# Performance work log

Hardware: AMD Instinct MI355X
Metric: run time of the kernel (lower is better)

Reference implementation:

```python
import jax, jax.numpy as jnp
import numpy as np

B, C, H, W = 2, 512, 48, 48
HEADS = 8
REDUCTION = 4
DPH = max(C // REDUCTION // HEADS, 1)   # 16
TOTAL = DPH * HEADS                      # 128
EPS_NORM = 1e-12
EPS_BN = 1e-5


def setup_inputs() -> dict:
    key = jax.random.key(0)
    ks = jax.random.split(key, 6)
    x = jax.random.normal(ks[0], (B, C, H, W), dtype=jnp.float32)
    # 1x1 convs stored as [out_ch, in_ch] matrices
    w_qkv = jax.random.normal(ks[1], (3 * TOTAL, C), dtype=jnp.float32) * (1.0 / np.sqrt(C))
    w_out = jax.random.normal(ks[2], (C, TOTAL), dtype=jnp.float32) * (1.0 / np.sqrt(TOTAL))
    temperature = jnp.ones((HEADS, 1, 1), dtype=jnp.float32)
    bn_gamma = jnp.ones((C,), dtype=jnp.float32)
    bn_beta = jnp.zeros((C,), dtype=jnp.float32)
    return {"x": x, "w_qkv": w_qkv, "temperature": temperature,
            "w_out": w_out, "bn_gamma": bn_gamma, "bn_beta": bn_beta}


def _l2norm(t):
    # F.normalize(t, dim=-1): t / max(||t||_2, eps)
    n = jnp.sqrt(jnp.sum(t * t, axis=-1, keepdims=True))
    return t / jnp.maximum(n, EPS_NORM)


def reference(x, w_qkv, temperature, w_out, bn_gamma, bn_beta):
    b, c, h, w = x.shape
    n = h * w
    # qkv 1x1 conv: [b, 3*TOTAL, h, w]
    qkv = jnp.einsum('bchw,oc->bohw', x, w_qkv)
    q, k, v = jnp.split(qkv, 3, axis=1)
    # [b, heads, dph, n] -> [b, heads, n, dph]
    def heads_tokens(t):
        return t.reshape(b, HEADS, DPH, n).transpose(0, 1, 3, 2)
    q = _l2norm(heads_tokens(q))
    k = _l2norm(heads_tokens(k))
    v = heads_tokens(v)
    # [b, heads, n, n]
    attn = jnp.einsum('bhnd,bhmd->bhnm', q, k) * temperature[None]
    attn = jax.nn.softmax(attn, axis=-1)
    out = jnp.einsum('bhnm,bhmd->bhnd', attn, v)          # [b, heads, n, dph]
    out = out.transpose(0, 1, 3, 2).reshape(b, TOTAL, h, w)
    # project_out: 1x1 conv then BatchNorm2d (training-mode batch stats)
    out = jnp.einsum('bthw,ct->bchw', out, w_out)
    mean = jnp.mean(out, axis=(0, 2, 3))
    var = jnp.mean((out - mean[None, :, None, None]) ** 2, axis=(0, 2, 3))
    out = (out - mean[None, :, None, None]) * jax.lax.rsqrt(var + EPS_BN)[None, :, None, None]
    out = out * bn_gamma[None, :, None, None] + bn_beta[None, :, None, None]
    return out
```

## Files before the change

kernel.cpp:

```cpp
#include <hip/hip_runtime.h>

#define NB 2
#define CC 512
#define NN 2304
#define NH 8
#define DD 16
#define TT 128
#define O3 384

typedef __attribute__((ext_vector_type(4))) float f32x4;
typedef __attribute__((ext_vector_type(8))) __bf16 bf16x8;
typedef __attribute__((ext_vector_type(4))) __bf16 bf16x4;
typedef __attribute__((ext_vector_type(4))) _Float16 f16x4;

__global__ __launch_bounds__(256) void k0_convert(
    const float* __restrict__ x, const float* __restrict__ wqkv,
    const float* __restrict__ wout,
    __bf16* __restrict__ xT, __bf16* __restrict__ wqb, __bf16* __restrict__ wob)
{
    int bid = blockIdx.x;
    int t = threadIdx.x;
    if (bid < 576) {
        __shared__ float tile[64][65];
        int b = bid / 288, rem = bid % 288;
        int nt = rem / 8, cb = rem % 8;
        int n0 = nt * 64, c0 = cb * 64;
        int tc = t >> 6, tn = t & 63;
#pragma unroll
        for (int i = 0; i < 16; i++) {
            int cl = i * 4 + tc;
            tile[cl][tn] = x[(size_t)(b * CC + c0 + cl) * NN + n0 + tn];
        }
        __syncthreads();
#pragma unroll
        for (int i = 0; i < 16; i++) {
            int nl = i * 4 + tc;
            xT[(size_t)(b * NN + n0 + nl) * CC + c0 + tn] = (__bf16)tile[tn][nl];
        }
    } else {
        int wid = bid - 576;
        int base = wid * 256 + t;
#pragma unroll
        for (int i = 0; i < 16; i++) {
            int j = base + i * 16384;
            if (j < O3 * CC) wqb[j] = (__bf16)wqkv[j];
            else             wob[j - O3 * CC] = (__bf16)wout[j - O3 * CC];
        }
    }
}

__global__ __launch_bounds__(256) void k1_qkv(
    const __bf16* __restrict__ xT, const __bf16* __restrict__ wqb,
    _Float16* __restrict__ Q, _Float16* __restrict__ K, _Float16* __restrict__ VT)
{
    int ob = blockIdx.x, nt = blockIdx.y, b = blockIdx.z;
    int lane = threadIdx.x & 63, wave = threadIdx.x >> 6;
    int quad = lane >> 4, col = lane & 15;
    int n0 = nt * 64 + wave * 16;
    int o0 = ob * 32;

    f32x4 acc[2];
    acc[0] = (f32x4){0.f, 0.f, 0.f, 0.f};
    acc[1] = (f32x4){0.f, 0.f, 0.f, 0.f};

    const __bf16* arow = xT + (size_t)(b * NN + n0 + col) * CC + quad * 8;
    const __bf16* brow0 = wqb + (size_t)(o0 + col) * CC + quad * 8;
    const __bf16* brow1 = brow0 + 16 * CC;

    bf16x8 a  = *(const bf16x8*)(arow);
    bf16x8 w0 = *(const bf16x8*)(brow0);
    bf16x8 w1 = *(const bf16x8*)(brow1);
#pragma unroll
    for (int ks = 0; ks < 16; ks++) {
        bf16x8 an, wn0, wn1;
        if (ks < 15) {
            an  = *(const bf16x8*)(arow + (ks + 1) * 32);
            wn0 = *(const bf16x8*)(brow0 + (ks + 1) * 32);
            wn1 = *(const bf16x8*)(brow1 + (ks + 1) * 32);
        }
        acc[0] = __builtin_amdgcn_mfma_f32_16x16x32_bf16(a, w0, acc[0], 0, 0, 0);
        acc[1] = __builtin_amdgcn_mfma_f32_16x16x32_bf16(a, w1, acc[1], 0, 0, 0);
        a = an; w0 = wn0; w1 = wn1;
    }

#pragma unroll
    for (int s = 0; s < 2; s++) {
        int oc = o0 + s * 16 + col;
        int d = oc & 15, h = (oc >> 4) & 7, kind = oc >> 7;
        f32x4 v = acc[s];
        if (kind < 2) {
            float ss0 = v[0] * v[0], ss1 = v[1] * v[1], ss2 = v[2] * v[2], ss3 = v[3] * v[3];
#pragma unroll
            for (int m = 1; m < 16; m <<= 1) {
                ss0 += __shfl_xor(ss0, m);
                ss1 += __shfl_xor(ss1, m);
                ss2 += __shfl_xor(ss2, m);
                ss3 += __shfl_xor(ss3, m);
            }
            v[0] *= 1.0f / fmaxf(sqrtf(ss0), 1e-12f);
            v[1] *= 1.0f / fmaxf(sqrtf(ss1), 1e-12f);
            v[2] *= 1.0f / fmaxf(sqrtf(ss2), 1e-12f);
            v[3] *= 1.0f / fmaxf(sqrtf(ss3), 1e-12f);
            _Float16* dst = (kind == 0 ? Q : K) + (size_t)(b * NH + h) * NN * DD;
#pragma unroll
            for (int r = 0; r < 4; r++) {
                int n = n0 + quad * 4 + r;
                dst[(size_t)n * DD + d] = (_Float16)v[r];
            }
        } else {
            f16x4 pk;
#pragma unroll
            for (int r = 0; r < 4; r++) pk[r] = (_Float16)v[r];
            int n = n0 + quad * 4;
            *(f16x4*)(VT + (size_t)((b * NH + h) * DD + d) * NN + n) = pk;
        }
    }
}

__global__ __launch_bounds__(512) void k2_attn(
    const _Float16* __restrict__ Q, const _Float16* __restrict__ K,
    const _Float16* __restrict__ VT, const float* __restrict__ temp,
    __bf16* __restrict__ AO)
{
    __shared__ float Osh[8][16][64];
    __shared__ float Lsh[8][64];

    int qt = blockIdx.x, bh = blockIdx.y;
    int lane = threadIdx.x & 63, wave = threadIdx.x >> 6;
    int quad = lane >> 4, col = lane & 15;
    int kbase = wave * 288;
    int qbase = qt * 64;

    const _Float16* Qb = Q + (size_t)bh * NN * DD;
    float tl2 = temp[bh & 7] * 1.4426950408889634f;

    f16x4 qf0 = *(const f16x4*)(Qb + (size_t)(qbase +  0 + col) * DD + quad * 4);
    f16x4 qf1 = *(const f16x4*)(Qb + (size_t)(qbase + 16 + col) * DD + quad * 4);
    f16x4 qf2 = *(const f16x4*)(Qb + (size_t)(qbase + 32 + col) * DD + quad * 4);
    f16x4 qf3 = *(const f16x4*)(Qb + (size_t)(qbase + 48 + col) * DD + quad * 4);

    f32x4 oa0 = {0.f,0.f,0.f,0.f}, oa1 = {0.f,0.f,0.f,0.f};
    f32x4 oa2 = {0.f,0.f,0.f,0.f}, oa3 = {0.f,0.f,0.f,0.f};
    float la0 = 0.f, la1 = 0.f, la2 = 0.f, la3 = 0.f;
    const f32x4 zc = {0.f,0.f,0.f,0.f};

    const _Float16* kp = K + (size_t)bh * NN * DD + (size_t)(kbase + col) * DD + quad * 4;
    const _Float16* vp = VT + (size_t)bh * DD * NN + (size_t)col * NN + kbase + quad * 4;

    f16x4 kfa = *(const f16x4*)(kp);
    f16x4 kfb = *(const f16x4*)(kp + 16 * DD);
    f16x4 vfa = *(const f16x4*)(vp);
    f16x4 vfb = *(const f16x4*)(vp + 16);

#define K2_CHUNK(KF, VF)                                                        \
    {                                                                           \
        f32x4 s0 = __builtin_amdgcn_mfma_f32_16x16x16f16(KF, qf0, zc, 0, 0, 0); \
        f32x4 s1 = __builtin_amdgcn_mfma_f32_16x16x16f16(KF, qf1, zc, 0, 0, 0); \
        f32x4 s2 = __builtin_amdgcn_mfma_f32_16x16x16f16(KF, qf2, zc, 0, 0, 0); \
        f32x4 s3 = __builtin_amdgcn_mfma_f32_16x16x16f16(KF, qf3, zc, 0, 0, 0); \
        f16x4 p0, p1, p2, p3;                                                   \
        _Pragma("unroll")                                                       \
        for (int r = 0; r < 4; ++r) {                                           \
            float e0 = __builtin_amdgcn_exp2f(tl2 * s0[r]);                     \
            float e1 = __builtin_amdgcn_exp2f(tl2 * s1[r]);                     \
            float e2 = __builtin_amdgcn_exp2f(tl2 * s2[r]);                     \
            float e3 = __builtin_amdgcn_exp2f(tl2 * s3[r]);                     \
            p0[r] = (_Float16)e0; la0 += e0;                                    \
            p1[r] = (_Float16)e1; la1 += e1;                                    \
            p2[r] = (_Float16)e2; la2 += e2;                                    \
            p3[r] = (_Float16)e3; la3 += e3;                                    \
        }                                                                       \
        oa0 = __builtin_amdgcn_mfma_f32_16x16x16f16(VF, p0, oa0, 0, 0, 0);      \
        oa1 = __builtin_amdgcn_mfma_f32_16x16x16f16(VF, p1, oa1, 0, 0, 0);      \
        oa2 = __builtin_amdgcn_mfma_f32_16x16x16f16(VF, p2, oa2, 0, 0, 0);      \
        oa3 = __builtin_amdgcn_mfma_f32_16x16x16f16(VF, p3, oa3, 0, 0, 0);      \
    }

    for (int g = 0; g < 9; ++g) {
        f16x4 kna, knb, vna, vnb;
        if (g < 8) {
            kna = *(const f16x4*)(kp + 32 * DD);
            knb = *(const f16x4*)(kp + 48 * DD);
            vna = *(const f16x4*)(vp + 32);
            vnb = *(const f16x4*)(vp + 48);
        }
        K2_CHUNK(kfa, vfa)
        K2_CHUNK(kfb, vfb)
        kfa = kna; kfb = knb; vfa = vna; vfb = vnb;
        kp += 32 * DD; vp += 32;
    }
#undef K2_CHUNK

    la0 += __shfl_xor(la0, 16); la0 += __shfl_xor(la0, 32);
    la1 += __shfl_xor(la1, 16); la1 += __shfl_xor(la1, 32);
    la2 += __shfl_xor(la2, 16); la2 += __shfl_xor(la2, 32);
    la3 += __shfl_xor(la3, 16); la3 += __shfl_xor(la3, 32);

#pragma unroll
    for (int r = 0; r < 4; ++r) {
        Osh[wave][quad * 4 + r][ 0 + col] = oa0[r];
        Osh[wave][quad * 4 + r][16 + col] = oa1[r];
        Osh[wave][quad * 4 + r][32 + col] = oa2[r];
        Osh[wave][quad * 4 + r][48 + col] = oa3[r];
    }
    float lv = (quad == 0) ? la0 : (quad == 1) ? la1 : (quad == 2) ? la2 : la3;
    Lsh[wave][quad * 16 + col] = lv;
    __syncthreads();

    int t = threadIdx.x;
    int q = t & 63, dg = t >> 6;
    float l = 0.f;
#pragma unroll
    for (int w = 0; w < 8; ++w) l += Lsh[w][q];
    float inv = 1.0f / l;
    float o0 = 0.f, o1 = 0.f;
#pragma unroll
    for (int w = 0; w < 8; ++w) {
        o0 += Osh[w][dg * 2 + 0][q];
        o1 += Osh[w][dg * 2 + 1][q];
    }
    int b = bh >> 3, h = bh & 7;
    __bf16* dst = AO + (size_t)(b * NN + qbase + q) * TT + h * DD + dg * 2;
    dst[0] = (__bf16)(o0 * inv);
    dst[1] = (__bf16)(o1 * inv);
}

__global__ __launch_bounds__(256) void k3_proj(
    const __bf16* __restrict__ AO, const __bf16* __restrict__ wob,
    float* __restrict__ out)
{
    int cb = blockIdx.x, nt = blockIdx.y, b = blockIdx.z;
    int lane = threadIdx.x & 63, wave = threadIdx.x >> 6;
    int quad = lane >> 4, col = lane & 15;
    int n0 = nt * 64 + wave * 16, c0 = cb * 32;

    f32x4 acc[2];
    acc[0] = (f32x4){0.f, 0.f, 0.f, 0.f};
    acc[1] = (f32x4){0.f, 0.f, 0.f, 0.f};

    const __bf16* ab = AO + (size_t)(b * NN + n0 + col) * TT + quad * 8;
    const __bf16* wb0 = wob + (size_t)(c0 + col) * TT + quad * 8;
    const __bf16* wb1 = wb0 + 16 * TT;
#pragma unroll
    for (int ks = 0; ks < 4; ks++) {
        bf16x8 a  = *(const bf16x8*)(ab + ks * 32);
        bf16x8 w0 = *(const bf16x8*)(wb0 + ks * 32);
        bf16x8 w1 = *(const bf16x8*)(wb1 + ks * 32);
        acc[0] = __builtin_amdgcn_mfma_f32_16x16x32_bf16(a, w0, acc[0], 0, 0, 0);
        acc[1] = __builtin_amdgcn_mfma_f32_16x16x32_bf16(a, w1, acc[1], 0, 0, 0);
    }
#pragma unroll
    for (int s = 0; s < 2; s++) {
        int c = c0 + s * 16 + col;
        float* dst = out + (size_t)(b * CC + c) * NN + n0 + quad * 4;
        *(f32x4*)dst = acc[s];
    }
}

__global__ __launch_bounds__(256) void k4_bn(
    float* __restrict__ out, const float* __restrict__ gamma,
    const float* __restrict__ beta)
{
    int c = blockIdx.x;
    int t = threadIdx.x;
    float vals[18];
    float s = 0.f, q = 0.f;
#pragma unroll
    for (int i = 0; i < 18; i++) {
        int j = i * 256 + t;
        int b = j / NN, n = j % NN;
        float v = out[(size_t)(b * CC + c) * NN + n];
        vals[i] = v; s += v; q += v * v;
    }
#pragma unroll
    for (int m = 1; m < 64; m <<= 1) { s += __shfl_xor(s, m); q += __shfl_xor(q, m); }
    __shared__ float rs[4], rq[4];
    int lane = t & 63, wave = t >> 6;
    if (lane == 0) { rs[wave] = s; rq[wave] = q; }
    __syncthreads();
    s = rs[0] + rs[1] + rs[2] + rs[3];
    q = rq[0] + rq[1] + rq[2] + rq[3];
    float mean = s * (1.0f / 4608.0f);
    float var = q * (1.0f / 4608.0f) - mean * mean;
    float sc = rsqrtf(var + 1e-5f) * gamma[c];
    float sh = beta[c] - mean * sc;
#pragma unroll
    for (int i = 0; i < 18; i++) {
        int j = i * 256 + t;
        int b = j / NN, n = j % NN;
        out[(size_t)(b * CC + c) * NN + n] = vals[i] * sc + sh;
    }
}

extern "C" void kernel_launch(void* const* d_in, const int* in_sizes, int n_in,
                              void* d_out, int out_size, void* d_ws, size_t ws_size,
                              hipStream_t stream) {
    const float* x     = (const float*)d_in[0];
    const float* wqkv  = (const float*)d_in[1];
    const float* temp  = (const float*)d_in[2];
    const float* wout  = (const float*)d_in[3];
    const float* gamma = (const float*)d_in[4];
    const float* beta  = (const float*)d_in[5];
    float* out = (float*)d_out;

    char* ws = (char*)d_ws;
    const size_t OFF_XT = 0;
    const size_t OFF_WQ = 4718592;
    const size_t OFF_WO = 5111808;
    const size_t OFF_Q  = 5242880;
    const size_t OFF_K  = 6422528;
    const size_t OFF_VT = 7602176;
    const size_t OFF_AO = 8781824;

    __bf16* xT  = (__bf16*)(ws + OFF_XT);
    __bf16* wqb = (__bf16*)(ws + OFF_WQ);
    __bf16* wob = (__bf16*)(ws + OFF_WO);
    _Float16* Q  = (_Float16*)(ws + OFF_Q);
    _Float16* K  = (_Float16*)(ws + OFF_K);
    _Float16* VT = (_Float16*)(ws + OFF_VT);
    __bf16* AO  = (__bf16*)(ws + OFF_AO);

    k0_convert<<<640, 256, 0, stream>>>(x, wqkv, wout, xT, wqb, wob);
    k1_qkv<<<dim3(12, 36, 2), 256, 0, stream>>>(xT, wqb, Q, K, VT);
    k2_attn<<<dim3(36, 16), 512, 0, stream>>>(Q, K, VT, temp, AO);
    k3_proj<<<dim3(16, 36, 2), 256, 0, stream>>>(AO, wob, out);
    k4_bn<<<512, 256, 0, stream>>>(out, gamma, beta);
}
```

Measured before the change: 138.2 us.

## Fuse all stages into one cooperative persistent kernel with grid syncs

Replaces the five separate launches with a single cooperative kernel that walks each stage's work units in a grid-stride loop, separated by grid.sync barriers. The goal is to remove per-launch overhead and inter-kernel gaps. The attention stage now uses 4 waves per 256-thread block, each covering twice as many keys, instead of 8 waves per block. The costs are grid-wide barrier latency, lower parallelism within each attention block, and occupancy limited by the shared-memory union. If the cooperative launch fails, it falls back to the original multi-kernel path.

```diff
diff --git a/kernel.cpp b/kernel.cpp
--- a/kernel.cpp
+++ b/kernel.cpp
@@ -1,4 +1,7 @@
 #include <hip/hip_runtime.h>
+#include <hip/hip_cooperative_groups.h>
+
+namespace cg = cooperative_groups;
 
 #define NB 2
 #define CC 512
@@ -13,144 +16,160 @@
 typedef __attribute__((ext_vector_type(4))) __bf16 bf16x4;
 typedef __attribute__((ext_vector_type(4))) _Float16 f16x4;
 
-__global__ __launch_bounds__(256) void k0_convert(
+#define OFF_XT 0u
+#define OFF_WQ 4718592u
+#define OFF_WO 5111808u
+#define OFF_Q  5242880u
+#define OFF_K  6422528u
+#define OFF_VT 7602176u
+#define OFF_AO 8781824u
+
+__global__ __launch_bounds__(256, 2) void mega(
     const float* __restrict__ x, const float* __restrict__ wqkv,
-    const float* __restrict__ wout,
-    __bf16* __restrict__ xT, __bf16* __restrict__ wqb, __bf16* __restrict__ wob)
+    const float* __restrict__ temp, const float* __restrict__ wout,
+    const float* __restrict__ gamma, const float* __restrict__ beta,
+    float* __restrict__ out, char* __restrict__ ws)
 {
-    int bid = blockIdx.x;
-    int t = threadIdx.x;
-    if (bid < 576) {
-        __shared__ float tile[64][65];
-        int b = bid / 288, rem = bid % 288;
-        int nt = rem / 8, cb = rem % 8;
-        int n0 = nt * 64, c0 = cb * 64;
-        int tc = t >> 6, tn = t & 63;
-#pragma unroll
-        for (int i = 0; i < 16; i++) {
-            int cl = i * 4 + tc;
-            tile[cl][tn] = x[(size_t)(b * CC + c0 + cl) * NN + n0 + tn];
+    __bf16*   xT  = (__bf16*)(ws + OFF_XT);
+    __bf16*   wqb = (__bf16*)(ws + OFF_WQ);
+    __bf16*   wob = (__bf16*)(ws + OFF_WO);
+    _Float16* Q   = (_Float16*)(ws + OFF_Q);
+    _Float16* K   = (_Float16*)(ws + OFF_K);
+    _Float16* VT  = (_Float16*)(ws + OFF_VT);
+    __bf16*   AO  = (__bf16*)(ws + OFF_AO);
+
+    __shared__ union {
+        float tile[64][65];
+        struct { float O[4][16][64]; float L[4][64]; } c;
+        struct { float rs[4]; float rq[4]; } e;
+    } sm;
+
+    cg::grid_group grid = cg::this_grid();
+    const int gsz = gridDim.x;
+    const int bid = blockIdx.x;
+    const int t = threadIdx.x;
+    const int lane = t & 63, wave = t >> 6;
+    const int quad = lane >> 4, col = lane & 15;
+
+    for (int u = bid; u < 640; u += gsz) {
+        if (u < 576) {
+            int b = u / 288, rem = u % 288;
+            int nt = rem / 8, cb = rem % 8;
+            int n0 = nt * 64, c0 = cb * 64;
+            int tc = t >> 6, tn = t & 63;
+#pragma unroll
+            for (int i = 0; i < 16; i++) {
+                int cl = i * 4 + tc;
+                sm.tile[cl][tn] = x[(size_t)(b * CC + c0 + cl) * NN + n0 + tn];
+            }
+            __syncthreads();
+#pragma unroll
+            for (int i = 0; i < 16; i++) {
+                int nl = i * 4 + tc;
+                xT[(size_t)(b * NN + n0 + nl) * CC + c0 + tn] = (__bf16)sm.tile[tn][nl];
+            }
+        } else {
+            int wid = u - 576;
+            int base = wid * 256 + t;
+#pragma unroll
+            for (int i = 0; i < 16; i++) {
+                int j = base + i * 16384;
+                if (j < O3 * CC) wqb[j] = (__bf16)wqkv[j];
+                else             wob[j - O3 * CC] = (__bf16)wout[j - O3 * CC];
+            }
         }
         __syncthreads();
-#pragma unroll
-        for (int i = 0; i < 16; i++) {
-            int nl = i * 4 + tc;
-            xT[(size_t)(b * NN + n0 + nl) * CC + c0 + tn] = (__bf16)tile[tn][nl];
-        }
-    } else {
-        int wid = bid - 576;
-        int base = wid * 256 + t;
-#pragma unroll
-        for (int i = 0; i < 16; i++) {
-            int j = base + i * 16384;
-            if (j < O3 * CC) wqb[j] = (__bf16)wqkv[j];
-            else             wob[j - O3 * CC] = (__bf16)wout[j - O3 * CC];
-        }
-    }
-}
-
-__global__ __launch_bounds__(256) void k1_qkv(
-    const __bf16* __restrict__ xT, const __bf16* __restrict__ wqb,
-    _Float16* __restrict__ Q, _Float16* __restrict__ K, _Float16* __restrict__ VT)
-{
-    int ob = blockIdx.x, nt = blockIdx.y, b = blockIdx.z;
-    int lane = threadIdx.x & 63, wave = threadIdx.x >> 6;
-    int quad = lane >> 4, col = lane & 15;
-    int n0 = nt * 64 + wave * 16;
-    int o0 = ob * 32;
-
-    f32x4 acc[2];
-    acc[0] = (f32x4){0.f, 0.f, 0.f, 0.f};
-    acc[1] = (f32x4){0.f, 0.f, 0.f, 0.f};
-
-    const __bf16* arow = xT + (size_t)(b * NN + n0 + col) * CC + quad * 8;
-    const __bf16* brow0 = wqb + (size_t)(o0 + col) * CC + quad * 8;
-    const __bf16* brow1 = brow0 + 16 * CC;
-
-    bf16x8 a  = *(const bf16x8*)(arow);
-    bf16x8 w0 = *(const bf16x8*)(brow0);
-    bf16x8 w1 = *(const bf16x8*)(brow1);
-#pragma unroll
-    for (int ks = 0; ks < 16; ks++) {
-        bf16x8 an, wn0, wn1;
-        if (ks < 15) {
-            an  = *(const bf16x8*)(arow + (ks + 1) * 32);
-            wn0 = *(const bf16x8*)(brow0 + (ks + 1) * 32);
-            wn1 = *(const bf16x8*)(brow1 + (ks + 1) * 32);
-        }
-        acc[0] = __builtin_amdgcn_mfma_f32_16x16x32_bf16(a, w0, acc[0], 0, 0, 0);
-        acc[1] = __builtin_amdgcn_mfma_f32_16x16x32_bf16(a, w1, acc[1], 0, 0, 0);
-        a = an; w0 = wn0; w1 = wn1;
-    }
-
-#pragma unroll
-    for (int s = 0; s < 2; s++) {
-        int oc = o0 + s * 16 + col;
-        int d = oc & 15, h = (oc >> 4) & 7, kind = oc >> 7;
-        f32x4 v = acc[s];
-        if (kind < 2) {
-            float ss0 = v[0] * v[0], ss1 = v[1] * v[1], ss2 = v[2] * v[2], ss3 = v[3] * v[3];
-#pragma unroll
-            for (int m = 1; m < 16; m <<= 1) {
-                ss0 += __shfl_xor(ss0, m);
-                ss1 += __shfl_xor(ss1, m);
-                ss2 += __shfl_xor(ss2, m);
-                ss3 += __shfl_xor(ss3, m);
-            }
-            v[0] *= 1.0f / fmaxf(sqrtf(ss0), 1e-12f);
-            v[1] *= 1.0f / fmaxf(sqrtf(ss1), 1e-12f);
-            v[2] *= 1.0f / fmaxf(sqrtf(ss2), 1e-12f);
-            v[3] *= 1.0f / fmaxf(sqrtf(ss3), 1e-12f);
-            _Float16* dst = (kind == 0 ? Q : K) + (size_t)(b * NH + h) * NN * DD;
-#pragma unroll
-            for (int r = 0; r < 4; r++) {
-                int n = n0 + quad * 4 + r;
-                dst[(size_t)n * DD + d] = (_Float16)v[r];
-            }
-        } else {
-            f16x4 pk;
-#pragma unroll
-            for (int r = 0; r < 4; r++) pk[r] = (_Float16)v[r];
-            int n = n0 + quad * 4;
-            *(f16x4*)(VT + (size_t)((b * NH + h) * DD + d) * NN + n) = pk;
-        }
-    }
-}
-
-__global__ __launch_bounds__(512) void k2_attn(
-    const _Float16* __restrict__ Q, const _Float16* __restrict__ K,
-    const _Float16* __restrict__ VT, const float* __restrict__ temp,
-    __bf16* __restrict__ AO)
-{
-    __shared__ float Osh[8][16][64];
-    __shared__ float Lsh[8][64];
-
-    int qt = blockIdx.x, bh = blockIdx.y;
-    int lane = threadIdx.x & 63, wave = threadIdx.x >> 6;
-    int quad = lane >> 4, col = lane & 15;
-    int kbase = wave * 288;
-    int qbase = qt * 64;
-
-    const _Float16* Qb = Q + (size_t)bh * NN * DD;
-    float tl2 = temp[bh & 7] * 1.4426950408889634f;
-
-    f16x4 qf0 = *(const f16x4*)(Qb + (size_t)(qbase +  0 + col) * DD + quad * 4);
-    f16x4 qf1 = *(const f16x4*)(Qb + (size_t)(qbase + 16 + col) * DD + quad * 4);
-    f16x4 qf2 = *(const f16x4*)(Qb + (size_t)(qbase + 32 + col) * DD + quad * 4);
-    f16x4 qf3 = *(const f16x4*)(Qb + (size_t)(qbase + 48 + col) * DD + quad * 4);
-
-    f32x4 oa0 = {0.f,0.f,0.f,0.f}, oa1 = {0.f,0.f,0.f,0.f};
-    f32x4 oa2 = {0.f,0.f,0.f,0.f}, oa3 = {0.f,0.f,0.f,0.f};
-    float la0 = 0.f, la1 = 0.f, la2 = 0.f, la3 = 0.f;
-    const f32x4 zc = {0.f,0.f,0.f,0.f};
-
-    const _Float16* kp = K + (size_t)bh * NN * DD + (size_t)(kbase + col) * DD + quad * 4;
-    const _Float16* vp = VT + (size_t)bh * DD * NN + (size_t)col * NN + kbase + quad * 4;
-
-    f16x4 kfa = *(const f16x4*)(kp);
-    f16x4 kfb = *(const f16x4*)(kp + 16 * DD);
-    f16x4 vfa = *(const f16x4*)(vp);
-    f16x4 vfb = *(const f16x4*)(vp + 16);
+    }
+    grid.sync();
+
+    for (int u = bid; u < 864; u += gsz) {
+        int ob = u % 12, nt = (u / 12) % 36, b = u / 432;
+        int n0 = nt * 64 + wave * 16;
+        int o0 = ob * 32;
+
+        f32x4 acc0 = {0.f, 0.f, 0.f, 0.f};
+        f32x4 acc1 = {0.f, 0.f, 0.f, 0.f};
+
+        const __bf16* arow  = xT + (size_t)(b * NN + n0 + col) * CC + quad * 8;
+        const __bf16* brow0 = wqb + (size_t)(o0 + col) * CC + quad * 8;
+        const __bf16* brow1 = brow0 + 16 * CC;
+
+        bf16x8 a  = *(const bf16x8*)(arow);
+        bf16x8 w0 = *(const bf16x8*)(brow0);
+        bf16x8 w1 = *(const bf16x8*)(brow1);
+#pragma unroll
+        for (int ks = 0; ks < 16; ks++) {
+            bf16x8 an, wn0, wn1;
+            if (ks < 15) {
+                an  = *(const bf16x8*)(arow + (ks + 1) * 32);
+                wn0 = *(const bf16x8*)(brow0 + (ks + 1) * 32);
+                wn1 = *(const bf16x8*)(brow1 + (ks + 1) * 32);
+            }
+            acc0 = __builtin_amdgcn_mfma_f32_16x16x32_bf16(a, w0, acc0, 0, 0, 0);
+            acc1 = __builtin_amdgcn_mfma_f32_16x16x32_bf16(a, w1, acc1, 0, 0, 0);
+            a = an; w0 = wn0; w1 = wn1;
+        }
+
+#pragma unroll
+        for (int s = 0; s < 2; s++) {
+            int oc = o0 + s * 16 + col;
+            int d = oc & 15, h = (oc >> 4) & 7, kind = oc >> 7;
+            f32x4 v = (s == 0) ? acc0 : acc1;
+            if (kind < 2) {
+                float ss0 = v[0] * v[0], ss1 = v[1] * v[1], ss2 = v[2] * v[2], ss3 = v[3] * v[3];
+#pragma unroll
+                for (int m = 1; m < 16; m <<= 1) {
+                    ss0 += __shfl_xor(ss0, m);
+                    ss1 += __shfl_xor(ss1, m);
+                    ss2 += __shfl_xor(ss2, m);
+                    ss3 += __shfl_xor(ss3, m);
+                }
+                v[0] *= 1.0f / fmaxf(sqrtf(ss0), 1e-12f);
+                v[1] *= 1.0f / fmaxf(sqrtf(ss1), 1e-12f);
+                v[2] *= 1.0f / fmaxf(sqrtf(ss2), 1e-12f);
+                v[3] *= 1.0f / fmaxf(sqrtf(ss3), 1e-12f);
+                _Float16* dst = (kind == 0 ? Q : K) + (size_t)(b * NH + h) * NN * DD;
+#pragma unroll
+                for (int r = 0; r < 4; r++) {
+                    int n = n0 + quad * 4 + r;
+                    dst[(size_t)n * DD + d] = (_Float16)v[r];
+                }
+            } else {
+                f16x4 pk;
+#pragma unroll
+                for (int r = 0; r < 4; r++) pk[r] = (_Float16)v[r];
+                int n = n0 + quad * 4;
+                *(f16x4*)(VT + (size_t)((b * NH + h) * DD + d) * NN + n) = pk;
+            }
+        }
+    }
+    grid.sync();
+
+    for (int u = bid; u < 576; u += gsz) {
+        int qt = u % 36, bh = u / 36;
+        int kbase = wave * 576;
+        int qbase = qt * 64;
+
+        const _Float16* Qb = Q + (size_t)bh * NN * DD;
+        float tl2 = temp[bh & 7] * 1.4426950408889634f;
+
+        f16x4 qf0 = *(const f16x4*)(Qb + (size_t)(qbase +  0 + col) * DD + quad * 4);
+        f16x4 qf1 = *(const f16x4*)(Qb + (size_t)(qbase + 16 + col) * DD + quad * 4);
+        f16x4 qf2 = *(const f16x4*)(Qb + (size_t)(qbase + 32 + col) * DD + quad * 4);
+        f16x4 qf3 = *(const f16x4*)(Qb + (size_t)(qbase + 48 + col) * DD + quad * 4);
+
+        f32x4 oa0 = {0.f,0.f,0.f,0.f}, oa1 = {0.f,0.f,0.f,0.f};
+        f32x4 oa2 = {0.f,0.f,0.f,0.f}, oa3 = {0.f,0.f,0.f,0.f};
+        float la0 = 0.f, la1 = 0.f, la2 = 0.f, la3 = 0.f;
+        const f32x4 zc = {0.f,0.f,0.f,0.f};
+
+        const _Float16* kp = K + (size_t)bh * NN * DD + (size_t)(kbase + col) * DD + quad * 4;
+        const _Float16* vp = VT + (size_t)bh * DD * NN + (size_t)col * NN + kbase + quad * 4;
+
+        f16x4 kfa = *(const f16x4*)(kp);
+        f16x4 kfb = *(const f16x4*)(kp + 16 * DD);
+        f16x4 vfa = *(const f16x4*)(vp);
+        f16x4 vfb = *(const f16x4*)(vp + 16);
 
 #define K2_CHUNK(KF, VF)                                                        \
     {                                                                           \
@@ -176,6 +195,282 @@
         oa3 = __builtin_amdgcn_mfma_f32_16x16x16f16(VF, p3, oa3, 0, 0, 0);      \
     }
 
+        for (int g = 0; g < 18; ++g) {
+            f16x4 kna, knb, vna, vnb;
+            if (g < 17) {
+                kna = *(const f16x4*)(kp + 32 * DD);
+                knb = *(const f16x4*)(kp + 48 * DD);
+                vna = *(const f16x4*)(vp + 32);
+                vnb = *(const f16x4*)(vp + 48);
+            }
+            K2_CHUNK(kfa, vfa)
+            K2_CHUNK(kfb, vfb)
+            kfa = kna; kfb = knb; vfa = vna; vfb = vnb;
+            kp += 32 * DD; vp += 32;
+        }
+#undef K2_CHUNK
+
+        la0 += __shfl_xor(la0, 16); la0 += __shfl_xor(la0, 32);
+        la1 += __shfl_xor(la1, 16); la1 += __shfl_xor(la1, 32);
+        la2 += __shfl_xor(la2, 16); la2 += __shfl_xor(la2, 32);
+        la3 += __shfl_xor(la3, 16); la3 += __shfl_xor(la3, 32);
+
+#pragma unroll
+        for (int r = 0; r < 4; ++r) {
+            sm.c.O[wave][quad * 4 + r][ 0 + col] = oa0[r];
+            sm.c.O[wave][quad * 4 + r][16 + col] = oa1[r];
+            sm.c.O[wave][quad * 4 + r][32 + col] = oa2[r];
+            sm.c.O[wave][quad * 4 + r][48 + col] = oa3[r];
+        }
+        float lv = (quad == 0) ? la0 : (quad == 1) ? la1 : (quad == 2) ? la2 : la3;
+        sm.c.L[wave][quad * 16 + col] = lv;
+        __syncthreads();
+
+        int q = t & 63, dg = t >> 6;
+        float l = 0.f;
+#pragma unroll
+        for (int w = 0; w < 4; ++w) l += sm.c.L[w][q];
+        float inv = 1.0f / l;
+        float o0 = 0.f, o1 = 0.f, o2 = 0.f, o3 = 0.f;
+#pragma unroll
+        for (int w = 0; w < 4; ++w) {
+            o0 += sm.c.O[w][dg * 4 + 0][q];
+            o1 += sm.c.O[w][dg * 4 + 1][q];
+            o2 += sm.c.O[w][dg * 4 + 2][q];
+            o3 += sm.c.O[w][dg * 4 + 3][q];
+        }
+        int b = bh >> 3, h = bh & 7;
+        bf16x4 pkv;
+        pkv[0] = (__bf16)(o0 * inv);
+        pkv[1] = (__bf16)(o1 * inv);
+        pkv[2] = (__bf16)(o2 * inv);
+        pkv[3] = (__bf16)(o3 * inv);
+        *(bf16x4*)(AO + (size_t)(b * NN + qbase + q) * TT + h * DD + dg * 4) = pkv;
+        __syncthreads();
+    }
+    grid.sync();
+
+    for (int u = bid; u < 1152; u += gsz) {
+        int cb = u % 16, nt = (u / 16) % 36, b = u / 576;
+        int n0 = nt * 64 + wave * 16, c0 = cb * 32;
+
+        f32x4 acc0 = {0.f, 0.f, 0.f, 0.f};
+        f32x4 acc1 = {0.f, 0.f, 0.f, 0.f};
+
+        const __bf16* ab  = AO + (size_t)(b * NN + n0 + col) * TT + quad * 8;
+        const __bf16* wb0 = wob + (size_t)(c0 + col) * TT + quad * 8;
+        const __bf16* wb1 = wb0 + 16 * TT;
+#pragma unroll
+        for (int ks = 0; ks < 4; ks++) {
+            bf16x8 a  = *(const bf16x8*)(ab + ks * 32);
+            bf16x8 w0 = *(const bf16x8*)(wb0 + ks * 32);
+            bf16x8 w1 = *(const bf16x8*)(wb1 + ks * 32);
+            acc0 = __builtin_amdgcn_mfma_f32_16x16x32_bf16(a, w0, acc0, 0, 0, 0);
+            acc1 = __builtin_amdgcn_mfma_f32_16x16x32_bf16(a, w1, acc1, 0, 0, 0);
+        }
+#pragma unroll
+        for (int s = 0; s < 2; s++) {
+            int c = c0 + s * 16 + col;
+            float* dst = out + (size_t)(b * CC + c) * NN + n0 + quad * 4;
+            *(f32x4*)dst = (s == 0) ? acc0 : acc1;
+        }
+    }
+    grid.sync();
+
+    for (int u = bid; u < 512; u += gsz) {
+        int c = u;
+        float vals[18];
+        float s = 0.f, q = 0.f;
+#pragma unroll
+        for (int i = 0; i < 18; i++) {
+            int j = i * 256 + t;
+            int b = j / NN, n = j % NN;
+            float v = out[(size_t)(b * CC + c) * NN + n];
+            vals[i] = v; s += v; q += v * v;
+        }
+#pragma unroll
+        for (int m = 1; m < 64; m <<= 1) { s += __shfl_xor(s, m); q += __shfl_xor(q, m); }
+        if (lane == 0) { sm.e.rs[wave] = s; sm.e.rq[wave] = q; }
+        __syncthreads();
+        s = sm.e.rs[0] + sm.e.rs[1] + sm.e.rs[2] + sm.e.rs[3];
+        q = sm.e.rq[0] + sm.e.rq[1] + sm.e.rq[2] + sm.e.rq[3];
+        float mean = s * (1.0f / 4608.0f);
+        float var  = q * (1.0f / 4608.0f) - mean * mean;
+        float sc = rsqrtf(var + 1e-5f) * gamma[c];
+        float sh = beta[c] - mean * sc;
+#pragma unroll
+        for (int i = 0; i < 18; i++) {
+            int j = i * 256 + t;
+            int b = j / NN, n = j % NN;
+            out[(size_t)(b * CC + c) * NN + n] = vals[i] * sc + sh;
+        }
+        __syncthreads();
+    }
+}
+
+__global__ __launch_bounds__(256) void k0_convert(
+    const float* __restrict__ x, const float* __restrict__ wqkv,
+    const float* __restrict__ wout,
+    __bf16* __restrict__ xT, __bf16* __restrict__ wqb, __bf16* __restrict__ wob)
+{
+    int bid = blockIdx.x;
+    int t = threadIdx.x;
+    if (bid < 576) {
+        __shared__ float tile[64][65];
+        int b = bid / 288, rem = bid % 288;
+        int nt = rem / 8, cb = rem % 8;
+        int n0 = nt * 64, c0 = cb * 64;
+        int tc = t >> 6, tn = t & 63;
+#pragma unroll
+        for (int i = 0; i < 16; i++) {
+            int cl = i * 4 + tc;
+            tile[cl][tn] = x[(size_t)(b * CC + c0 + cl) * NN + n0 + tn];
+        }
+        __syncthreads();
+#pragma unroll
+        for (int i = 0; i < 16; i++) {
+            int nl = i * 4 + tc;
+            xT[(size_t)(b * NN + n0 + nl) * CC + c0 + tn] = (__bf16)tile[tn][nl];
+        }
+    } else {
+        int wid = bid - 576;
+        int base = wid * 256 + t;
+#pragma unroll
+        for (int i = 0; i < 16; i++) {
+            int j = base + i * 16384;
+            if (j < O3 * CC) wqb[j] = (__bf16)wqkv[j];
+            else             wob[j - O3 * CC] = (__bf16)wout[j - O3 * CC];
+        }
+    }
+}
+
+__global__ __launch_bounds__(256) void k1_qkv(
+    const __bf16* __restrict__ xT, const __bf16* __restrict__ wqb,
+    _Float16* __restrict__ Q, _Float16* __restrict__ K, _Float16* __restrict__ VT)
+{
+    int ob = blockIdx.x, nt = blockIdx.y, b = blockIdx.z;
+    int lane = threadIdx.x & 63, wave = threadIdx.x >> 6;
+    int quad = lane >> 4, col = lane & 15;
+    int n0 = nt * 64 + wave * 16;
+    int o0 = ob * 32;
+
+    f32x4 acc[2];
+    acc[0] = (f32x4){0.f, 0.f, 0.f, 0.f};
+    acc[1] = (f32x4){0.f, 0.f, 0.f, 0.f};
+
+    const __bf16* arow = xT + (size_t)(b * NN + n0 + col) * CC + quad * 8;
+    const __bf16* brow0 = wqb + (size_t)(o0 + col) * CC + quad * 8;
+    const __bf16* brow1 = brow0 + 16 * CC;
+
+    bf16x8 a  = *(const bf16x8*)(arow);
+    bf16x8 w0 = *(const bf16x8*)(brow0);
+    bf16x8 w1 = *(const bf16x8*)(brow1);
+#pragma unroll
+    for (int ks = 0; ks < 16; ks++) {
+        bf16x8 an, wn0, wn1;
+        if (ks < 15) {
+            an  = *(const bf16x8*)(arow + (ks + 1) * 32);
+            wn0 = *(const bf16x8*)(brow0 + (ks + 1) * 32);
+            wn1 = *(const bf16x8*)(brow1 + (ks + 1) * 32);
+        }
+        acc[0] = __builtin_amdgcn_mfma_f32_16x16x32_bf16(a, w0, acc[0], 0, 0, 0);
+        acc[1] = __builtin_amdgcn_mfma_f32_16x16x32_bf16(a, w1, acc[1], 0, 0, 0);
+        a = an; w0 = wn0; w1 = wn1;
+    }
+
+#pragma unroll
+    for (int s = 0; s < 2; s++) {
+        int oc = o0 + s * 16 + col;
+        int d = oc & 15, h = (oc >> 4) & 7, kind = oc >> 7;
+        f32x4 v = acc[s];
+        if (kind < 2) {
+            float ss0 = v[0] * v[0], ss1 = v[1] * v[1], ss2 = v[2] * v[2], ss3 = v[3] * v[3];
+#pragma unroll
+            for (int m = 1; m < 16; m <<= 1) {
+                ss0 += __shfl_xor(ss0, m);
+                ss1 += __shfl_xor(ss1, m);
+                ss2 += __shfl_xor(ss2, m);
+                ss3 += __shfl_xor(ss3, m);
+            }
+            v[0] *= 1.0f / fmaxf(sqrtf(ss0), 1e-12f);
+            v[1] *= 1.0f / fmaxf(sqrtf(ss1), 1e-12f);
+            v[2] *= 1.0f / fmaxf(sqrtf(ss2), 1e-12f);
+            v[3] *= 1.0f / fmaxf(sqrtf(ss3), 1e-12f);
+            _Float16* dst = (kind == 0 ? Q : K) + (size_t)(b * NH + h) * NN * DD;
+#pragma unroll
+            for (int r = 0; r < 4; r++) {
+                int n = n0 + quad * 4 + r;
+                dst[(size_t)n * DD + d] = (_Float16)v[r];
+            }
+        } else {
+            f16x4 pk;
+#pragma unroll
+            for (int r = 0; r < 4; r++) pk[r] = (_Float16)v[r];
+            int n = n0 + quad * 4;
+            *(f16x4*)(VT + (size_t)((b * NH + h) * DD + d) * NN + n) = pk;
+        }
+    }
+}
+
+__global__ __launch_bounds__(512) void k2_attn(
+    const _Float16* __restrict__ Q, const _Float16* __restrict__ K,
+    const _Float16* __restrict__ VT, const float* __restrict__ temp,
+    __bf16* __restrict__ AO)
+{
+    __shared__ float Osh[8][16][64];
+    __shared__ float Lsh[8][64];
+
+    int qt = blockIdx.x, bh = blockIdx.y;
+    int lane = threadIdx.x & 63, wave = threadIdx.x >> 6;
+    int quad = lane >> 4, col = lane & 15;
+    int kbase = wave * 288;
+    int qbase = qt * 64;
+
+    const _Float16* Qb = Q + (size_t)bh * NN * DD;
+    float tl2 = temp[bh & 7] * 1.4426950408889634f;
+
+    f16x4 qf0 = *(const f16x4*)(Qb + (size_t)(qbase +  0 + col) * DD + quad * 4);
+    f16x4 qf1 = *(const f16x4*)(Qb + (size_t)(qbase + 16 + col) * DD + quad * 4);
+    f16x4 qf2 = *(const f16x4*)(Qb + (size_t)(qbase + 32 + col) * DD + quad * 4);
+    f16x4 qf3 = *(const f16x4*)(Qb + (size_t)(qbase + 48 + col) * DD + quad * 4);
+
+    f32x4 oa0 = {0.f,0.f,0.f,0.f}, oa1 = {0.f,0.f,0.f,0.f};
+    f32x4 oa2 = {0.f,0.f,0.f,0.f}, oa3 = {0.f,0.f,0.f,0.f};
+    float la0 = 0.f, la1 = 0.f, la2 = 0.f, la3 = 0.f;
+    const f32x4 zc = {0.f,0.f,0.f,0.f};
+
+    const _Float16* kp = K + (size_t)bh * NN * DD + (size_t)(kbase + col) * DD + quad * 4;
+    const _Float16* vp = VT + (size_t)bh * DD * NN + (size_t)col * NN + kbase + quad * 4;
+
+    f16x4 kfa = *(const f16x4*)(kp);
+    f16x4 kfb = *(const f16x4*)(kp + 16 * DD);
+    f16x4 vfa = *(const f16x4*)(vp);
+    f16x4 vfb = *(const f16x4*)(vp + 16);
+
+#define K2_CHUNK(KF, VF)                                                        \
+    {                                                                           \
+        f32x4 s0 = __builtin_amdgcn_mfma_f32_16x16x16f16(KF, qf0, zc, 0, 0, 0); \
+        f32x4 s1 = __builtin_amdgcn_mfma_f32_16x16x16f16(KF, qf1, zc, 0, 0, 0); \
+        f32x4 s2 = __builtin_amdgcn_mfma_f32_16x16x16f16(KF, qf2, zc, 0, 0, 0); \
+        f32x4 s3 = __builtin_amdgcn_mfma_f32_16x16x16f16(KF, qf3, zc, 0, 0, 0); \
+        f16x4 p0, p1, p2, p3;                                                   \
+        _Pragma("unroll")                                                       \
+        for (int r = 0; r < 4; ++r) {                                           \
+            float e0 = __builtin_amdgcn_exp2f(tl2 * s0[r]);                     \
+            float e1 = __builtin_amdgcn_exp2f(tl2 * s1[r]);                     \
+            float e2 = __builtin_amdgcn_exp2f(tl2 * s2[r]);                     \
+            float e3 = __builtin_amdgcn_exp2f(tl2 * s3[r]);                     \
+            p0[r] = (_Float16)e0; la0 += e0;                                    \
+            p1[r] = (_Float16)e1; la1 += e1;                                    \
+            p2[r] = (_Float16)e2; la2 += e2;                                    \
+            p3[r] = (_Float16)e3; la3 += e3;                                    \
+        }                                                                       \
+        oa0 = __builtin_amdgcn_mfma_f32_16x16x16f16(VF, p0, oa0, 0, 0, 0);      \
+        oa1 = __builtin_amdgcn_mfma_f32_16x16x16f16(VF, p1, oa1, 0, 0, 0);      \
+        oa2 = __builtin_amdgcn_mfma_f32_16x16x16f16(VF, p2, oa2, 0, 0, 0);      \
+        oa3 = __builtin_amdgcn_mfma_f32_16x16x16f16(VF, p3, oa3, 0, 0, 0);      \
+    }
+
     for (int g = 0; g < 9; ++g) {
         f16x4 kna, knb, vna, vnb;
         if (g < 8) {
@@ -302,15 +597,25 @@
     const float* gamma = (const float*)d_in[4];
     const float* beta  = (const float*)d_in[5];
     float* out = (float*)d_out;
-
     char* ws = (char*)d_ws;
-    const size_t OFF_XT = 0;
-    const size_t OFF_WQ = 4718592;
-    const size_t OFF_WO = 5111808;
-    const size_t OFF_Q  = 5242880;
-    const size_t OFF_K  = 6422528;
-    const size_t OFF_VT = 7602176;
-    const size_t OFF_AO = 8781824;
+
+    static int coop_blocks_per_cu = -1;
+    if (coop_blocks_per_cu < 0) {
+        int nb = 0;
+        hipError_t qe = hipOccupancyMaxActiveBlocksPerMultiprocessor(
+            &nb, (const void*)mega, 256, 0);
+        coop_blocks_per_cu = (qe == hipSuccess && nb > 0) ? nb : 0;
+    }
+
+    if (coop_blocks_per_cu > 0) {
+        int gsz = coop_blocks_per_cu * 256;
+        if (gsz > 1152) gsz = 1152;
+        void* args[] = {(void*)&x, (void*)&wqkv, (void*)&temp, (void*)&wout,
+                        (void*)&gamma, (void*)&beta, (void*)&out, (void*)&ws};
+        hipError_t e = hipLaunchCooperativeKernel((const void*)mega, dim3(gsz),
+                                                  dim3(256), args, 0, stream);
+        if (e == hipSuccess) return;
+    }
 
     __bf16* xT  = (__bf16*)(ws + OFF_XT);
     __bf16* wqb = (__bf16*)(ws + OFF_WQ);
```

After: 386.5 us. 180% more time.
